# Performance work log

Hardware: AMD Instinct MI355X
Metric: run time of the kernel (lower is better)

The kernel has to match this reference:

```python
import jax, jax.numpy as jnp
import numpy as np

N = 500_000   # mesh vertices
M = 500_000   # non-manifold sample points
K = 4         # quad-mesh valence
WEIGHTS = [7000.0, 600.0, 10.0, 50.0, 30.0, 3.0]


def setup_inputs() -> dict:
    key = jax.random.key(0)
    ks = jax.random.split(key, 11)
    return {
        "manifold_pred": jax.random.normal(ks[0], (1, N), jnp.float32),
        "nonmanifold_pred": jax.random.normal(ks[1], (1, M), jnp.float32),
        "mnfld_grad": jax.random.normal(ks[2], (1, N, 3), jnp.float32),
        "nonmnfld_grad": jax.random.normal(ks[3], (1, M, 3), jnp.float32),
        "mnfld_hessian": jax.random.normal(ks[4], (1, N, 3, 3), jnp.float32),
        "mnfld_n_gt": jax.random.normal(ks[5], (1, N, 3), jnp.float32),
        "theta": jax.random.normal(ks[6], (1, N, 1), jnp.float32),
        "local_coord_u": jax.random.normal(ks[7], (1, N, 3), jnp.float32),
        "local_coord_v": jax.random.normal(ks[8], (1, N, 3), jnp.float32),
        "rot": jax.random.normal(ks[9], (N, K, 3, 3), jnp.float32),
        "neighbors": jax.random.randint(ks[10], (N, K), 0, N, jnp.int32),
    }


def reference(manifold_pred, nonmanifold_pred, mnfld_grad, nonmnfld_grad,
              mnfld_hessian, mnfld_n_gt, theta, local_coord_u, local_coord_v,
              rot, neighbors):
    H = mnfld_hessian[0]          # [N,3,3] per-vertex hessian
    n_gt = mnfld_n_gt[0]          # [N,3]

    # morse term: n^T H  (div_type == 'l1')
    morse = 0.5 * jnp.abs(jnp.einsum('nd,nde->ne', n_gt, H)).mean()

    sdf_term = jnp.abs(manifold_pred).mean()

    # eikonal over concatenated grads (morse path uses nonmnfld_grad when near_points is None)
    all_grads = jnp.concatenate([nonmnfld_grad, mnfld_grad], axis=-2)  # [1, M+N, 3]
    eikonal_term = jnp.abs(jnp.linalg.norm(all_grads, axis=2) - 1.0).mean()

    inter_term = jnp.exp(-100.0 * jnp.abs(nonmanifold_pred)).mean()

    # cross-field directions from theta
    u, v, th = local_coord_u[0], local_coord_v[0], theta[0]  # [N,3],[N,3],[N,1]
    va = u * jnp.cos(th) + v * jnp.sin(th)
    va = va / (jnp.linalg.norm(va, axis=-1, keepdims=True) + 1e-12)
    vb = -u * jnp.sin(th) + v * jnp.cos(th)
    vb = vb / (jnp.linalg.norm(vb, axis=-1, keepdims=True) + 1e-12)

    # per-vertex (v^T H) x v hessian alignment (single valence group covers all vertices)
    vaH = jnp.einsum('nd,nde->ne', va, H)
    vbH = jnp.einsum('nd,nde->ne', vb, H)
    h_alpha = jnp.abs(jnp.cross(vaH, va)).mean()
    h_beta = jnp.abs(jnp.cross(vbH, vb)).mean()
    theta_hessian_term = 0.5 * (h_alpha + h_beta)

    # neighbor consistency: rotate neighbor cross-field into vertex frame, dot products
    vaj = jnp.einsum('nkij,nkj->nki', rot, va[neighbors])  # [N,K,3]
    vbj = jnp.einsum('nkij,nkj->nki', rot, vb[neighbors])
    aa = jnp.abs(jnp.einsum('nd,nkd->nk', va, vaj))
    ab = jnp.abs(jnp.einsum('nd,nkd->nk', va, vbj))
    ba = jnp.abs(jnp.einsum('nd,nkd->nk', vb, vaj))
    bb = jnp.abs(jnp.einsum('nd,nkd->nk', vb, vbj))
    theta_neighbors_term = (aa + ab + ba + bb - 2.0).mean()

    w = WEIGHTS
    loss = (w[0] * sdf_term + w[1] * inter_term + w[3] * eikonal_term
            + w[5] * morse + w[2] * theta_hessian_term + w[4] * theta_neighbors_term)
    return jnp.stack([loss, sdf_term, inter_term, eikonal_term, morse,
                      theta_hessian_term, theta_neighbors_term])
```

## Files before the change

### kernel.cpp

```cpp
#include <hip/hip_runtime.h>
#include <math.h>

static constexpr int BLOCK = 256;
static constexpr int WAVES = BLOCK / 64;
static constexpr int KVAL = 4;
static constexpr int TILE = 256;

typedef float f4 __attribute__((ext_vector_type(4)));
typedef int i4 __attribute__((ext_vector_type(4)));
typedef unsigned int u4v __attribute__((ext_vector_type(4)));
union VV { u4v u4; _Float16 h[8]; };
union PQ { u4v u[3]; _Float16 h[24]; };

__device__ __forceinline__ void norm3(float x, float y, float z,
                                      float& ox, float& oy, float& oz) {
  float inv = 1.0f / (sqrtf(x * x + y * y + z * z) + 1e-12f);
  ox = x * inv; oy = y * inv; oz = z * inv;
}

template <int NV>
__device__ __forceinline__ void block_reduce(float (&p)[NV]) {
#pragma unroll
  for (int off = 32; off > 0; off >>= 1)
#pragma unroll
    for (int q = 0; q < NV; ++q) p[q] += __shfl_down(p[q], off, 64);
  __shared__ float sm[WAVES][NV];
  int wave = threadIdx.x >> 6, lane = threadIdx.x & 63;
  if (lane == 0)
#pragma unroll
    for (int q = 0; q < NV; ++q) sm[wave][q] = p[q];
  __syncthreads();
  if (threadIdx.x == 0) {
#pragma unroll
    for (int q = 0; q < NV; ++q) {
      float t = 0.f;
#pragma unroll
      for (int w = 1; w < WAVES; ++w) t += sm[w][q];
      p[q] += t;
    }
  }
}

__device__ __forceinline__ void stage_f(float* __restrict__ dst,
                                        const float* __restrict__ src, int nf) {
  int t = threadIdx.x;
  int nf4 = nf >> 2;
  const f4* s4 = (const f4*)src;
  f4* d4 = (f4*)dst;
  for (int i = t; i < nf4; i += BLOCK) d4[i] = s4[i];
  int rem = nf & 3;
  if (t < rem) dst[nf4 * 4 + t] = src[nf4 * 4 + t];
}

__global__ __launch_bounds__(BLOCK) void s1_kernel(
    const float* __restrict__ theta, const float* __restrict__ u,
    const float* __restrict__ v, u4v* __restrict__ vavb,
    u4v* __restrict__ pq0, u4v* __restrict__ pq1, u4v* __restrict__ pq2, int N,
    const float* __restrict__ pred, const float* __restrict__ pgrad,
    const float* __restrict__ mp, const float* __restrict__ grad,
    const float* __restrict__ H, const float* __restrict__ ngt,
    const float* __restrict__ rot,
    float* __restrict__ part1, int nb1, int M) {
  __shared__ float B[4608];
  int t = threadIdx.x;
  long base = (long)blockIdx.x * TILE;
  float p[5] = {0.f, 0.f, 0.f, 0.f, 0.f};

  int cntM = 0, cntN = 0;
  if (base < M) { long c = (long)M - base; cntM = c > TILE ? TILE : (int)c; }
  if (base < N) { long c = (long)N - base; cntN = c > TILE ? TILE : (int)c; }

  float prv = 0.f, mpv = 0.f, thv = 0.f;
  if (t < cntM) prv = pred[base + t];
  if (t < cntN) { mpv = mp[base + t]; thv = theta[base + t]; }

  if (cntM > 0) stage_f(B, pgrad + 3 * base, 3 * cntM);
  if (cntN > 0) {
    stage_f(B + 768, grad + 3 * base, 3 * cntN);
    stage_f(B + 1536, ngt + 3 * base, 3 * cntN);
  }
  __syncthreads();
  float ng0 = 0.f, ng1 = 0.f, ng2 = 0.f;
  if (t < cntM) {
    float gx = B[3 * t], gy = B[3 * t + 1], gz = B[3 * t + 2];
    p[1] += fabsf(sqrtf(gx * gx + gy * gy + gz * gz) - 1.0f);
    p[4] += __expf(-100.0f * fabsf(prv));
  }
  if (t < cntN) {
    float gx = B[768 + 3 * t], gy = B[768 + 3 * t + 1], gz = B[768 + 3 * t + 2];
    p[1] += fabsf(sqrtf(gx * gx + gy * gy + gz * gz) - 1.0f);
    p[0] = fabsf(mpv);
    ng0 = B[1536 + 3 * t]; ng1 = B[1536 + 3 * t + 1]; ng2 = B[1536 + 3 * t + 2];
  }
  __syncthreads();

  if (cntN > 0) {
    stage_f(B, u + 3 * base, 3 * cntN);
    stage_f(B + 768, v + 3 * base, 3 * cntN);
  }
  __syncthreads();
  float va[3] = {0.f, 0.f, 0.f}, vb[3] = {0.f, 0.f, 0.f};
  if (t < cntN) {
    float s, c;
    __sincosf(thv, &s, &c);
    float ux = B[3 * t], uy = B[3 * t + 1], uz = B[3 * t + 2];
    float vx = B[768 + 3 * t], vy = B[768 + 3 * t + 1], vz = B[768 + 3 * t + 2];
    norm3(ux * c + vx * s, uy * c + vy * s, uz * c + vz * s, va[0], va[1], va[2]);
    norm3(vx * c - ux * s, vy * c - uy * s, vz * c - uz * s, vb[0], vb[1], vb[2]);
    VV o;
    o.h[0] = (_Float16)va[0]; o.h[1] = (_Float16)va[1]; o.h[2] = (_Float16)va[2];
    o.h[3] = (_Float16)vb[0]; o.h[4] = (_Float16)vb[1]; o.h[5] = (_Float16)vb[2];
    o.h[6] = (_Float16)0.f;   o.h[7] = (_Float16)0.f;
    vavb[base + t] = o.u4;
  }
  __syncthreads();

  if (cntN > 0) stage_f(B, H + 9 * base, 9 * cntN);
  __syncthreads();
  if (t < cntN) {
    float h[9];
#pragma unroll
    for (int q = 0; q < 9; ++q) h[q] = B[9 * t + q];
    p[2] = fabsf(ng0 * h[0] + ng1 * h[3] + ng2 * h[6]) +
           fabsf(ng0 * h[1] + ng1 * h[4] + ng2 * h[7]) +
           fabsf(ng0 * h[2] + ng1 * h[5] + ng2 * h[8]);
    float a0 = va[0] * h[0] + va[1] * h[3] + va[2] * h[6];
    float a1 = va[0] * h[1] + va[1] * h[4] + va[2] * h[7];
    float a2 = va[0] * h[2] + va[1] * h[5] + va[2] * h[8];
    float b0 = vb[0] * h[0] + vb[1] * h[3] + vb[2] * h[6];
    float b1 = vb[0] * h[1] + vb[1] * h[4] + vb[2] * h[7];
    float b2 = vb[0] * h[2] + vb[1] * h[5] + vb[2] * h[8];
    p[3] = fabsf(a1 * va[2] - a2 * va[1]) + fabsf(a2 * va[0] - a0 * va[2]) +
           fabsf(a0 * va[1] - a1 * va[0]) + fabsf(b1 * vb[2] - b2 * vb[1]) +
           fabsf(b2 * vb[0] - b0 * vb[2]) + fabsf(b0 * vb[1] - b1 * vb[0]);
  }
  __syncthreads();

#pragma unroll
  for (int sp = 0; sp < 2; ++sp) {
    int cs = cntN - 128 * sp;
    if (cs < 0) cs = 0;
    if (cs > 128) cs = 128;
    if (cs > 0) stage_f(B, rot + 36 * (base + 128 * sp), 36 * cs);
    __syncthreads();
    int lt = t - 128 * sp;
    if (lt >= 0 && lt < cs) {
      long i = base + t;
      const float* R0 = B + 36 * lt;
      PQ o2;
#pragma unroll
      for (int k = 0; k < KVAL; ++k) {
        float R[9];
#pragma unroll
        for (int q = 0; q < 9; ++q) R[q] = R0[9 * k + q];
#pragma unroll
        for (int j = 0; j < 3; ++j) {
          float pa = R[j] * va[0] + R[3 + j] * va[1] + R[6 + j] * va[2];
          float pb = R[j] * vb[0] + R[3 + j] * vb[1] + R[6 + j] * vb[2];
          o2.h[6 * k + j] = (_Float16)pa;
          o2.h[6 * k + 3 + j] = (_Float16)pb;
        }
      }
      pq0[i] = o2.u[0]; pq1[i] = o2.u[1]; pq2[i] = o2.u[2];
    }
    __syncthreads();
  }

  block_reduce<5>(p);
  if (t == 0) {
#pragma unroll
    for (int q = 0; q < 5; ++q) part1[q * nb1 + blockIdx.x] = p[q];
  }
}

__global__ __launch_bounds__(BLOCK) void s3_kernel(
    const u4v* __restrict__ vavb, const u4v* __restrict__ pq0,
    const u4v* __restrict__ pq1, const u4v* __restrict__ pq2,
    const i4* __restrict__ nbr, float* __restrict__ part2, int N) {
  int n = blockIdx.x * BLOCK + threadIdx.x;
  float p[1] = {0.f};
  if (n < N) {
    i4 jj = nbr[n];
    int js[4] = {jj.x, jj.y, jj.z, jj.w};
    VV wn[4];
#pragma unroll
    for (int k = 0; k < KVAL; ++k) wn[k].u4 = vavb[js[k]];
    PQ o;
    o.u[0] = pq0[n]; o.u[1] = pq1[n]; o.u[2] = pq2[n];
    float nsum = 0.f;
#pragma unroll
    for (int k = 0; k < KVAL; ++k) {
      float pa0 = (float)o.h[6 * k],     pa1 = (float)o.h[6 * k + 1],
            pa2 = (float)o.h[6 * k + 2];
      float pb0 = (float)o.h[6 * k + 3], pb1 = (float)o.h[6 * k + 4],
            pb2 = (float)o.h[6 * k + 5];
      float aj0 = (float)wn[k].h[0], aj1 = (float)wn[k].h[1], aj2 = (float)wn[k].h[2];
      float bj0 = (float)wn[k].h[3], bj1 = (float)wn[k].h[4], bj2 = (float)wn[k].h[5];
      nsum += fabsf(pa0 * aj0 + pa1 * aj1 + pa2 * aj2) +
              fabsf(pa0 * bj0 + pa1 * bj1 + pa2 * bj2) +
              fabsf(pb0 * aj0 + pb1 * aj1 + pb2 * aj2) +
              fabsf(pb0 * bj0 + pb1 * bj1 + pb2 * bj2) - 2.0f;
    }
    p[0] = nsum;
  }
  block_reduce<1>(p);
  if (threadIdx.x == 0) part2[blockIdx.x] = p[0];
}

__global__ __launch_bounds__(BLOCK) void finalize_fast(
    const float* __restrict__ part1, int nb1, const float* __restrict__ part2,
    int nb2, float* __restrict__ out, int N, int M) {
  float s[6] = {0.f, 0.f, 0.f, 0.f, 0.f, 0.f};
  for (int b = threadIdx.x; b < nb1; b += BLOCK) {
#pragma unroll
    for (int q = 0; q < 5; ++q) s[q] += part1[q * nb1 + b];
  }
  for (int b = threadIdx.x; b < nb2; b += BLOCK) s[5] += part2[b];
  block_reduce<6>(s);
  if (threadIdx.x == 0) {
    float sdf = s[0] / (float)N;
    float eik = s[1] / (float)(N + M);
    float morse = 0.5f * s[2] / (3.0f * (float)N);
    float th = 0.5f * s[3] / (3.0f * (float)N);
    float inter = s[4] / (float)M;
    float nb = s[5] / ((float)N * (float)KVAL);
    float loss = 7000.0f * sdf + 600.0f * inter + 50.0f * eik + 3.0f * morse +
                 10.0f * th + 30.0f * nb;
    out[0] = loss; out[1] = sdf; out[2] = inter; out[3] = eik;
    out[4] = morse; out[5] = th; out[6] = nb;
  }
}

__device__ __forceinline__ void crossfield(const float* __restrict__ u,
                                           const float* __restrict__ v,
                                           const float* __restrict__ theta,
                                           int n, float va[3], float vb[3]) {
  float s, c;
  __sincosf(theta[n], &s, &c);
  float ux = u[3 * n], uy = u[3 * n + 1], uz = u[3 * n + 2];
  float vx = v[3 * n], vy = v[3 * n + 1], vz = v[3 * n + 2];
  norm3(ux * c + vx * s, uy * c + vy * s, uz * c + vz * s, va[0], va[1], va[2]);
  norm3(vx * c - ux * s, vy * c - uy * s, vz * c - uz * s, vb[0], vb[1], vb[2]);
}

__global__ __launch_bounds__(BLOCK) void vertex_kernel(
    const float* __restrict__ mp, const float* __restrict__ grad,
    const float* __restrict__ H, const float* __restrict__ ngt,
    const float* __restrict__ theta, const float* __restrict__ u,
    const float* __restrict__ v, const float* __restrict__ rot,
    const int* __restrict__ nbr, float* __restrict__ acc, int N) {
  int n = blockIdx.x * blockDim.x + threadIdx.x;
  float p[5] = {0.f, 0.f, 0.f, 0.f, 0.f};
  if (n < N) {
    float hh[9];
#pragma unroll
    for (int i = 0; i < 9; ++i) hh[i] = H[9 * (size_t)n + i];
    p[0] = fabsf(mp[n]);
    float gx = grad[3 * n], gy = grad[3 * n + 1], gz = grad[3 * n + 2];
    p[1] = fabsf(sqrtf(gx * gx + gy * gy + gz * gz) - 1.0f);
    float n0 = ngt[3 * n], n1 = ngt[3 * n + 1], n2 = ngt[3 * n + 2];
    p[2] = fabsf(n0 * hh[0] + n1 * hh[3] + n2 * hh[6]) +
           fabsf(n0 * hh[1] + n1 * hh[4] + n2 * hh[7]) +
           fabsf(n0 * hh[2] + n1 * hh[5] + n2 * hh[8]);
    float va[3], vb[3];
    crossfield(u, v, theta, n, va, vb);
    {
      float a0 = va[0] * hh[0] + va[1] * hh[3] + va[2] * hh[6];
      float a1 = va[0] * hh[1] + va[1] * hh[4] + va[2] * hh[7];
      float a2 = va[0] * hh[2] + va[1] * hh[5] + va[2] * hh[8];
      float b0 = vb[0] * hh[0] + vb[1] * hh[3] + vb[2] * hh[6];
      float b1 = vb[0] * hh[1] + vb[1] * hh[4] + vb[2] * hh[7];
      float b2 = vb[0] * hh[2] + vb[1] * hh[5] + vb[2] * hh[8];
      p[3] = fabsf(a1 * va[2] - a2 * va[1]) + fabsf(a2 * va[0] - a0 * va[2]) +
             fabsf(a0 * va[1] - a1 * va[0]) + fabsf(b1 * vb[2] - b2 * vb[1]) +
             fabsf(b2 * vb[0] - b0 * vb[2]) + fabsf(b0 * vb[1] - b1 * vb[0]);
    }
    float nsum = 0.f;
    const float* R = rot + (size_t)n * (KVAL * 9);
#pragma unroll
    for (int k = 0; k < KVAL; ++k) {
      int j = nbr[KVAL * (size_t)n + k];
      float vaj[3], vbj[3];
      crossfield(u, v, theta, j, vaj, vbj);
      float r0 = R[9 * k + 0], r1 = R[9 * k + 1], r2 = R[9 * k + 2];
      float r3 = R[9 * k + 3], r4 = R[9 * k + 4], r5 = R[9 * k + 5];
      float r6 = R[9 * k + 6], r7 = R[9 * k + 7], r8 = R[9 * k + 8];
      float wa0 = r0 * vaj[0] + r1 * vaj[1] + r2 * vaj[2];
      float wa1 = r3 * vaj[0] + r4 * vaj[1] + r5 * vaj[2];
      float wa2 = r6 * vaj[0] + r7 * vaj[1] + r8 * vaj[2];
      float wb0 = r0 * vbj[0] + r1 * vbj[1] + r2 * vbj[2];
      float wb1 = r3 * vbj[0] + r4 * vbj[1] + r5 * vbj[2];
      float wb2 = r6 * vbj[0] + r7 * vbj[1] + r8 * vbj[2];
      nsum += fabsf(va[0] * wa0 + va[1] * wa1 + va[2] * wa2) +
              fabsf(va[0] * wb0 + va[1] * wb1 + va[2] * wb2) +
              fabsf(vb[0] * wa0 + vb[1] * wa1 + vb[2] * wa2) +
              fabsf(vb[0] * wb0 + vb[1] * wb1 + vb[2] * wb2) - 2.0f;
    }
    p[4] = nsum;
  }
  block_reduce<5>(p);
  if (threadIdx.x == 0) {
    atomicAdd(&acc[0], p[0]); atomicAdd(&acc[1], p[1]); atomicAdd(&acc[2], p[2]);
    atomicAdd(&acc[3], p[3]); atomicAdd(&acc[4], p[4]);
  }
}

__global__ __launch_bounds__(BLOCK) void point_kernel(
    const float* __restrict__ pred, const float* __restrict__ grad,
    float* __restrict__ acc, int M) {
  int i = blockIdx.x * blockDim.x + threadIdx.x;
  float p[2] = {0.f, 0.f};
  if (i < M) {
    p[0] = __expf(-100.0f * fabsf(pred[i]));
    float gx = grad[3 * i], gy = grad[3 * i + 1], gz = grad[3 * i + 2];
    p[1] = fabsf(sqrtf(gx * gx + gy * gy + gz * gz) - 1.0f);
  }
  block_reduce<2>(p);
  if (threadIdx.x == 0) {
    atomicAdd(&acc[5], p[0]); atomicAdd(&acc[1], p[1]);
  }
}

__global__ void finalize_acc(const float* __restrict__ acc, float* __restrict__ out,
                             int N, int M) {
  if (threadIdx.x == 0 && blockIdx.x == 0) {
    float sdf = acc[0] / (float)N;
    float eik = acc[1] / (float)(N + M);
    float morse = 0.5f * acc[2] / (3.0f * (float)N);
    float th = 0.5f * acc[3] / (3.0f * (float)N);
    float nb = acc[4] / ((float)N * (float)KVAL);
    float inter = acc[5] / (float)M;
    float loss = 7000.0f * sdf + 600.0f * inter + 50.0f * eik + 3.0f * morse +
                 10.0f * th + 30.0f * nb;
    out[0] = loss; out[1] = sdf; out[2] = inter; out[3] = eik;
    out[4] = morse; out[5] = th; out[6] = nb;
  }
}

extern "C" void kernel_launch(void* const* d_in, const int* in_sizes, int n_in,
                              void* d_out, int out_size, void* d_ws, size_t ws_size,
                              hipStream_t stream) {
  const float* mp    = (const float*)d_in[0];
  const float* npred = (const float*)d_in[1];
  const float* grad  = (const float*)d_in[2];
  const float* ngrad = (const float*)d_in[3];
  const float* H     = (const float*)d_in[4];
  const float* ngt   = (const float*)d_in[5];
  const float* theta = (const float*)d_in[6];
  const float* u     = (const float*)d_in[7];
  const float* v     = (const float*)d_in[8];
  const float* rot   = (const float*)d_in[9];
  const int*   nbr   = (const int*)d_in[10];
  float* out = (float*)d_out;

  int N = in_sizes[0];
  int M = in_sizes[1];
  int mx = (N > M) ? N : M;
  int nb1 = (mx + TILE - 1) / TILE;
  int nb2 = (N + BLOCK - 1) / BLOCK;

  size_t off_vavb = 256;
  size_t off_pq0 = off_vavb + (size_t)N * 16;
  size_t off_pq1 = off_pq0 + (size_t)N * 16;
  size_t off_pq2 = off_pq1 + (size_t)N * 16;
  size_t off_p1 = off_pq2 + (size_t)N * 16;
  size_t off_p2 = off_p1 + (size_t)5 * nb1 * 4;
  size_t need = off_p2 + (size_t)nb2 * 4;

  if (ws_size >= need) {
    u4v* vavb    = (u4v*)((char*)d_ws + off_vavb);
    u4v* pq0     = (u4v*)((char*)d_ws + off_pq0);
    u4v* pq1     = (u4v*)((char*)d_ws + off_pq1);
    u4v* pq2     = (u4v*)((char*)d_ws + off_pq2);
    float* part1 = (float*)((char*)d_ws + off_p1);
    float* part2 = (float*)((char*)d_ws + off_p2);
    s1_kernel<<<nb1, BLOCK, 0, stream>>>(
        theta, u, v, vavb, pq0, pq1, pq2, N, npred, ngrad, mp, grad, H, ngt,
        rot, part1, nb1, M);
    s3_kernel<<<nb2, BLOCK, 0, stream>>>(
        vavb, pq0, pq1, pq2, (const i4*)nbr, part2, N);
    finalize_fast<<<1, BLOCK, 0, stream>>>(part1, nb1, part2, nb2, out, N, M);
  } else {
    float* acc = (float*)d_ws;
    (void)hipMemsetAsync(acc, 0, 6 * sizeof(float), stream);
    vertex_kernel<<<(N + BLOCK - 1) / BLOCK, BLOCK, 0, stream>>>(
        mp, grad, H, ngt, theta, u, v, rot, nbr, acc, N);
    point_kernel<<<(M + BLOCK - 1) / BLOCK, BLOCK, 0, stream>>>(npred, ngrad, acc, M);
    finalize_acc<<<1, 64, 0, stream>>>(acc, out, N, M);
  }
}
```

Measured before the change: 63.70 us.

## Move rotation products into neighbor kernel, dropping pq intermediate buffers

The rotation-matrix products are now computed in the second kernel, which reads rot directly and combines it with the gathered neighbor cross-fields. The three fp16 pq intermediate arrays are no longer written and read back, saving about 96 bytes of traffic per vertex. The first kernel's shared buffer shrinks by staging the gradient arrays one after another, which may raise occupancy at the cost of one extra barrier. The vavb stores now use nontemporal hints, and the second kernel has to read rot (144 B per vertex) after the first kernel instead of inside it.

```diff
diff --git a/kernel.cpp b/kernel.cpp
--- a/kernel.cpp
+++ b/kernel.cpp
@@ -10,7 +10,10 @@
 typedef int i4 __attribute__((ext_vector_type(4)));
 typedef unsigned int u4v __attribute__((ext_vector_type(4)));
 union VV { u4v u4; _Float16 h[8]; };
-union PQ { u4v u[3]; _Float16 h[24]; };
+
+__device__ __forceinline__ void nts4(u4v* p, u4v v) {
+  __builtin_nontemporal_store(v, p);
+}
 
 __device__ __forceinline__ void norm3(float x, float y, float z,
                                       float& ox, float& oy, float& oz) {
@@ -54,14 +57,12 @@
 
 __global__ __launch_bounds__(BLOCK) void s1_kernel(
     const float* __restrict__ theta, const float* __restrict__ u,
-    const float* __restrict__ v, u4v* __restrict__ vavb,
-    u4v* __restrict__ pq0, u4v* __restrict__ pq1, u4v* __restrict__ pq2, int N,
+    const float* __restrict__ v, u4v* __restrict__ vavb, int N,
     const float* __restrict__ pred, const float* __restrict__ pgrad,
     const float* __restrict__ mp, const float* __restrict__ grad,
     const float* __restrict__ H, const float* __restrict__ ngt,
-    const float* __restrict__ rot,
     float* __restrict__ part1, int nb1, int M) {
-  __shared__ float B[4608];
+  __shared__ float B[2304];
   int t = threadIdx.x;
   long base = (long)blockIdx.x * TILE;
   float p[5] = {0.f, 0.f, 0.f, 0.f, 0.f};
@@ -75,22 +76,24 @@
   if (t < cntN) { mpv = mp[base + t]; thv = theta[base + t]; }
 
   if (cntM > 0) stage_f(B, pgrad + 3 * base, 3 * cntM);
-  if (cntN > 0) {
-    stage_f(B + 768, grad + 3 * base, 3 * cntN);
-    stage_f(B + 1536, ngt + 3 * base, 3 * cntN);
-  }
-  __syncthreads();
-  float ng0 = 0.f, ng1 = 0.f, ng2 = 0.f;
+  __syncthreads();
   if (t < cntM) {
     float gx = B[3 * t], gy = B[3 * t + 1], gz = B[3 * t + 2];
     p[1] += fabsf(sqrtf(gx * gx + gy * gy + gz * gz) - 1.0f);
     p[4] += __expf(-100.0f * fabsf(prv));
   }
+  __syncthreads();
+  float ng0 = 0.f, ng1 = 0.f, ng2 = 0.f;
+  if (cntN > 0) {
+    stage_f(B, grad + 3 * base, 3 * cntN);
+    stage_f(B + 768, ngt + 3 * base, 3 * cntN);
+  }
+  __syncthreads();
   if (t < cntN) {
-    float gx = B[768 + 3 * t], gy = B[768 + 3 * t + 1], gz = B[768 + 3 * t + 2];
+    float gx = B[3 * t], gy = B[3 * t + 1], gz = B[3 * t + 2];
     p[1] += fabsf(sqrtf(gx * gx + gy * gy + gz * gz) - 1.0f);
     p[0] = fabsf(mpv);
-    ng0 = B[1536 + 3 * t]; ng1 = B[1536 + 3 * t + 1]; ng2 = B[1536 + 3 * t + 2];
+    ng0 = B[768 + 3 * t]; ng1 = B[768 + 3 * t + 1]; ng2 = B[768 + 3 * t + 2];
   }
   __syncthreads();
 
@@ -111,7 +114,7 @@
     o.h[0] = (_Float16)va[0]; o.h[1] = (_Float16)va[1]; o.h[2] = (_Float16)va[2];
     o.h[3] = (_Float16)vb[0]; o.h[4] = (_Float16)vb[1]; o.h[5] = (_Float16)vb[2];
     o.h[6] = (_Float16)0.f;   o.h[7] = (_Float16)0.f;
-    vavb[base + t] = o.u4;
+    nts4(&vavb[base + t], o.u4);
   }
   __syncthreads();
 
@@ -134,8 +137,39 @@
            fabsf(a0 * va[1] - a1 * va[0]) + fabsf(b1 * vb[2] - b2 * vb[1]) +
            fabsf(b2 * vb[0] - b0 * vb[2]) + fabsf(b0 * vb[1] - b1 * vb[0]);
   }
-  __syncthreads();
-
+
+  block_reduce<5>(p);
+  if (t == 0) {
+#pragma unroll
+    for (int q = 0; q < 5; ++q) part1[q * nb1 + blockIdx.x] = p[q];
+  }
+}
+
+__global__ __launch_bounds__(BLOCK) void s3_kernel(
+    const u4v* __restrict__ vavb, const float* __restrict__ rot,
+    const i4* __restrict__ nbr, float* __restrict__ part2, int N) {
+  __shared__ float B[4608];
+  int t = threadIdx.x;
+  long base = (long)blockIdx.x * TILE;
+  int cntN = 0;
+  if (base < N) { long c = (long)N - base; cntN = c > TILE ? TILE : (int)c; }
+  float p[1] = {0.f};
+
+  VV wn[4]; VV ws;
+  ws.u4 = u4v{0, 0, 0, 0};
+#pragma unroll
+  for (int k = 0; k < KVAL; ++k) wn[k].u4 = u4v{0, 0, 0, 0};
+  if (t < cntN) {
+    i4 jj = nbr[base + t];
+    int js[4] = {jj.x, jj.y, jj.z, jj.w};
+#pragma unroll
+    for (int k = 0; k < KVAL; ++k) wn[k].u4 = vavb[js[k]];
+    ws.u4 = vavb[base + t];
+  }
+  float va[3] = {(float)ws.h[0], (float)ws.h[1], (float)ws.h[2]};
+  float vb[3] = {(float)ws.h[3], (float)ws.h[4], (float)ws.h[5]};
+
+  float nsum = 0.f;
 #pragma unroll
   for (int sp = 0; sp < 2; ++sp) {
     int cs = cntN - 128 * sp;
@@ -145,66 +179,33 @@
     __syncthreads();
     int lt = t - 128 * sp;
     if (lt >= 0 && lt < cs) {
-      long i = base + t;
       const float* R0 = B + 36 * lt;
-      PQ o2;
 #pragma unroll
       for (int k = 0; k < KVAL; ++k) {
         float R[9];
 #pragma unroll
         for (int q = 0; q < 9; ++q) R[q] = R0[9 * k + q];
-#pragma unroll
-        for (int j = 0; j < 3; ++j) {
-          float pa = R[j] * va[0] + R[3 + j] * va[1] + R[6 + j] * va[2];
-          float pb = R[j] * vb[0] + R[3 + j] * vb[1] + R[6 + j] * vb[2];
-          o2.h[6 * k + j] = (_Float16)pa;
-          o2.h[6 * k + 3 + j] = (_Float16)pb;
-        }
+        float pa0 = R[0] * va[0] + R[3] * va[1] + R[6] * va[2];
+        float pa1 = R[1] * va[0] + R[4] * va[1] + R[7] * va[2];
+        float pa2 = R[2] * va[0] + R[5] * va[1] + R[8] * va[2];
+        float pb0 = R[0] * vb[0] + R[3] * vb[1] + R[6] * vb[2];
+        float pb1 = R[1] * vb[0] + R[4] * vb[1] + R[7] * vb[2];
+        float pb2 = R[2] * vb[0] + R[5] * vb[1] + R[8] * vb[2];
+        float aj0 = (float)wn[k].h[0], aj1 = (float)wn[k].h[1],
+              aj2 = (float)wn[k].h[2];
+        float bj0 = (float)wn[k].h[3], bj1 = (float)wn[k].h[4],
+              bj2 = (float)wn[k].h[5];
+        nsum += fabsf(pa0 * aj0 + pa1 * aj1 + pa2 * aj2) +
+                fabsf(pa0 * bj0 + pa1 * bj1 + pa2 * bj2) +
+                fabsf(pb0 * aj0 + pb1 * aj1 + pb2 * aj2) +
+                fabsf(pb0 * bj0 + pb1 * bj1 + pb2 * bj2) - 2.0f;
       }
-      pq0[i] = o2.u[0]; pq1[i] = o2.u[1]; pq2[i] = o2.u[2];
     }
     __syncthreads();
   }
-
-  block_reduce<5>(p);
-  if (t == 0) {
-#pragma unroll
-    for (int q = 0; q < 5; ++q) part1[q * nb1 + blockIdx.x] = p[q];
-  }
-}
-
-__global__ __launch_bounds__(BLOCK) void s3_kernel(
-    const u4v* __restrict__ vavb, const u4v* __restrict__ pq0,
-    const u4v* __restrict__ pq1, const u4v* __restrict__ pq2,
-    const i4* __restrict__ nbr, float* __restrict__ part2, int N) {
-  int n = blockIdx.x * BLOCK + threadIdx.x;
-  float p[1] = {0.f};
-  if (n < N) {
-    i4 jj = nbr[n];
-    int js[4] = {jj.x, jj.y, jj.z, jj.w};
-    VV wn[4];
-#pragma unroll
-    for (int k = 0; k < KVAL; ++k) wn[k].u4 = vavb[js[k]];
-    PQ o;
-    o.u[0] = pq0[n]; o.u[1] = pq1[n]; o.u[2] = pq2[n];
-    float nsum = 0.f;
-#pragma unroll
-    for (int k = 0; k < KVAL; ++k) {
-      float pa0 = (float)o.h[6 * k],     pa1 = (float)o.h[6 * k + 1],
-            pa2 = (float)o.h[6 * k + 2];
-      float pb0 = (float)o.h[6 * k + 3], pb1 = (float)o.h[6 * k + 4],
-            pb2 = (float)o.h[6 * k + 5];
-      float aj0 = (float)wn[k].h[0], aj1 = (float)wn[k].h[1], aj2 = (float)wn[k].h[2];
-      float bj0 = (float)wn[k].h[3], bj1 = (float)wn[k].h[4], bj2 = (float)wn[k].h[5];
-      nsum += fabsf(pa0 * aj0 + pa1 * aj1 + pa2 * aj2) +
-              fabsf(pa0 * bj0 + pa1 * bj1 + pa2 * bj2) +
-              fabsf(pb0 * aj0 + pb1 * aj1 + pb2 * aj2) +
-              fabsf(pb0 * bj0 + pb1 * bj1 + pb2 * bj2) - 2.0f;
-    }
-    p[0] = nsum;
-  }
+  p[0] = nsum;
   block_reduce<1>(p);
-  if (threadIdx.x == 0) part2[blockIdx.x] = p[0];
+  if (t == 0) part2[blockIdx.x] = p[0];
 }
 
 __global__ __launch_bounds__(BLOCK) void finalize_fast(
@@ -357,28 +358,21 @@
   int M = in_sizes[1];
   int mx = (N > M) ? N : M;
   int nb1 = (mx + TILE - 1) / TILE;
-  int nb2 = (N + BLOCK - 1) / BLOCK;
+  int nb2 = (N + TILE - 1) / TILE;
 
   size_t off_vavb = 256;
-  size_t off_pq0 = off_vavb + (size_t)N * 16;
-  size_t off_pq1 = off_pq0 + (size_t)N * 16;
-  size_t off_pq2 = off_pq1 + (size_t)N * 16;
-  size_t off_p1 = off_pq2 + (size_t)N * 16;
+  size_t off_p1 = off_vavb + (size_t)N * 16;
   size_t off_p2 = off_p1 + (size_t)5 * nb1 * 4;
   size_t need = off_p2 + (size_t)nb2 * 4;
 
   if (ws_size >= need) {
     u4v* vavb    = (u4v*)((char*)d_ws + off_vavb);
-    u4v* pq0     = (u4v*)((char*)d_ws + off_pq0);
-    u4v* pq1     = (u4v*)((char*)d_ws + off_pq1);
-    u4v* pq2     = (u4v*)((char*)d_ws + off_pq2);
     float* part1 = (float*)((char*)d_ws + off_p1);
     float* part2 = (float*)((char*)d_ws + off_p2);
     s1_kernel<<<nb1, BLOCK, 0, stream>>>(
-        theta, u, v, vavb, pq0, pq1, pq2, N, npred, ngrad, mp, grad, H, ngt,
-        rot, part1, nb1, M);
+        theta, u, v, vavb, N, npred, ngrad, mp, grad, H, ngt, part1, nb1, M);
     s3_kernel<<<nb2, BLOCK, 0, stream>>>(
-        vavb, pq0, pq1, pq2, (const i4*)nbr, part2, N);
+        vavb, rot, (const i4*)nbr, part2, N);
     finalize_fast<<<1, BLOCK, 0, stream>>>(part1, nb1, part2, nb2, out, N, M);
   } else {
     float* acc = (float*)d_ws;
```

New measurement: 59.84 us. 6.1% less time.
